# Performance work log

Measured on AMD Instinct MI355X. Metric: run time of the kernel, lower is better.

The kernel has to match this reference:

```python
import jax, jax.numpy as jnp
import numpy as np

NUM_USERS = 100000
NUM_ITEMS = 50000
EMB = 64
N_LAYERS = 3
N_EDGES = 2400000
NEG_SLOPE = 0.01  # torch F.leaky_relu default
EPS = 1e-12       # torch F.normalize default eps


def setup_inputs() -> dict:
    key = jax.random.key(0)
    ks = jax.random.split(key, 9)
    N = NUM_USERS + NUM_ITEMS
    adj_rows = jax.random.randint(ks[0], (N_EDGES,), 0, N, dtype=jnp.int32)
    adj_cols = jax.random.randint(ks[1], (N_EDGES,), 0, N, dtype=jnp.int32)
    # normalized adjacency values are small positive numbers
    adj_vals = jax.random.uniform(ks[2], (N_EDGES,), dtype=jnp.float32) * 0.01
    user_emb = jax.random.normal(ks[3], (NUM_USERS, EMB), dtype=jnp.float32) * 0.1
    item_emb = jax.random.normal(ks[4], (NUM_ITEMS, EMB), dtype=jnp.float32) * 0.1
    gc_w = jax.random.normal(ks[5], (N_LAYERS, EMB, EMB), dtype=jnp.float32) * 0.05
    gc_b = jax.random.normal(ks[6], (N_LAYERS, EMB), dtype=jnp.float32) * 0.01
    bi_w = jax.random.normal(ks[7], (N_LAYERS, EMB, EMB), dtype=jnp.float32) * 0.05
    bi_b = jax.random.normal(ks[8], (N_LAYERS, EMB), dtype=jnp.float32) * 0.01
    return {"adj_rows": adj_rows, "adj_cols": adj_cols, "adj_vals": adj_vals,
            "user_emb": user_emb, "item_emb": item_emb,
            "gc_w": gc_w, "gc_b": gc_b, "bi_w": bi_w, "bi_b": bi_b}


def reference(adj_rows, adj_cols, adj_vals, user_emb, item_emb, gc_w, gc_b, bi_w, bi_b):
    n_users = user_emb.shape[0]
    N = n_users + item_emb.shape[0]
    ego = jnp.concatenate([user_emb, item_emb], axis=0)  # [N, d]
    all_emb = [ego]
    n_layers = gc_w.shape[0]
    for i in range(n_layers):
        # SpMM: side = norm_adj @ ego  (COO gather-scale-scatter)
        side = jax.ops.segment_sum(adj_vals[:, None] * ego[adj_cols],
                                   adj_rows, num_segments=N)  # [N, d]
        sum_emb = jax.nn.leaky_relu(side @ gc_w[i] + gc_b[i], NEG_SLOPE)
        bi_emb = jax.nn.leaky_relu((ego * side) @ bi_w[i] + bi_b[i], NEG_SLOPE)
        ego = sum_emb + bi_emb  # dropout p=0 -> identity (eval mode)
        norm = ego / jnp.maximum(
            jnp.linalg.norm(ego, axis=1, keepdims=True), EPS)
        all_emb.append(norm)
    all_emb = jnp.concatenate(all_emb, axis=1)  # [N, d*(1+L)]
    return all_emb[:n_users], all_emb[n_users:]
```

## Files before the change

### kernel.cpp

```cpp
#include <hip/hip_runtime.h>
#include <hip/hip_bf16.h>

#define NUSERS 100000
#define NITEMS 50000
#define NNODES 150000
#define EMB 64
#define NLAYERS 3
#define NEDGES 2400000
#define SCAN_ITEMS 1024
#define NSCAN_BLOCKS ((NNODES + SCAN_ITEMS - 1) / SCAN_ITEMS)
#define NTILES (NNODES / 16)

typedef __attribute__((ext_vector_type(8))) short short8;
typedef __attribute__((ext_vector_type(4))) float float4v;

__device__ __forceinline__ float bf2f(unsigned short u) {
    return __uint_as_float((unsigned int)u << 16);
}
__device__ __forceinline__ unsigned short f2bf(float f) {
    unsigned int x = __float_as_uint(f);
    return (unsigned short)((x + 0x7FFFu + ((x >> 16) & 1u)) >> 16);
}


__global__ __launch_bounds__(256) void hist_rank_kernel(
    const int* __restrict__ rows, int* __restrict__ deg, int* __restrict__ rank)
{
    int e = blockIdx.x * 256 + threadIdx.x;
    if (e >= NEDGES) return;
    rank[e] = atomicAdd(&deg[rows[e]], 1);
}

__global__ __launch_bounds__(256) void block_sum_kernel(
    const int* __restrict__ deg, int* __restrict__ bsum)
{
    __shared__ int lds[256];
    int t = threadIdx.x;
    int base = blockIdx.x * SCAN_ITEMS + t * 4;
    int s = 0;
    #pragma unroll
    for (int k = 0; k < 4; ++k) {
        int idx = base + k;
        s += (idx < NNODES) ? deg[idx] : 0;
    }
    lds[t] = s; __syncthreads();
    for (int off = 128; off; off >>= 1) {
        if (t < off) lds[t] += lds[t + off];
        __syncthreads();
    }
    if (t == 0) bsum[blockIdx.x] = lds[0];
}

__global__ __launch_bounds__(256) void scan_partials_kernel(
    const int* __restrict__ bsum, int* __restrict__ bscan, int* __restrict__ rowptr)
{
    __shared__ int lds[256];
    int t = threadIdx.x;
    int v = (t < NSCAN_BLOCKS) ? bsum[t] : 0;
    lds[t] = v; __syncthreads();
    for (int off = 1; off < 256; off <<= 1) {
        int add = (t >= off) ? lds[t - off] : 0;
        __syncthreads();
        lds[t] += add;
        __syncthreads();
    }
    if (t < NSCAN_BLOCKS) bscan[t] = lds[t] - v;
    if (t == 0) rowptr[NNODES] = NEDGES;
}

__global__ __launch_bounds__(256) void block_scan_kernel(
    const int* __restrict__ deg, const int* __restrict__ bscan,
    int* __restrict__ rowptr)
{
    __shared__ int lds[256];
    int t = threadIdx.x;
    int base = blockIdx.x * SCAN_ITEMS + t * 4;
    int d[4]; int s = 0;
    #pragma unroll
    for (int k = 0; k < 4; ++k) {
        int idx = base + k;
        d[k] = (idx < NNODES) ? deg[idx] : 0;
        s += d[k];
    }
    lds[t] = s; __syncthreads();
    int v = s;
    for (int off = 1; off < 256; off <<= 1) {
        int add = (t >= off) ? lds[t - off] : 0;
        __syncthreads();
        lds[t] += add;
        __syncthreads();
    }
    int ex = lds[t] - v + bscan[blockIdx.x];
    #pragma unroll
    for (int k = 0; k < 4; ++k) {
        int idx = base + k;
        if (idx < NNODES) { rowptr[idx] = ex; ex += d[k]; }
    }
}

__global__ __launch_bounds__(256) void scatter_kernel(
    const int* __restrict__ rows, const int* __restrict__ cols,
    const float* __restrict__ vals, const int* __restrict__ rank,
    const int* __restrict__ rowptr, int2* __restrict__ edges)
{
    int e = blockIdx.x * 256 + threadIdx.x;
    if (e >= NEDGES) return;
    int pos = rowptr[rows[e]] + rank[e];
    edges[pos] = make_int2(cols[e], __float_as_int(vals[e]));
}

__global__ __launch_bounds__(256) void wconv_kernel(
    const float* __restrict__ gw, const float* __restrict__ bw,
    unsigned short* __restrict__ wg_bf, unsigned short* __restrict__ wb_bf)
{
    int i = blockIdx.x * 256 + threadIdx.x;
    if (i >= NLAYERS * EMB * EMB) return;
    int l = i >> 12;
    int k = (i >> 6) & 63;
    int n = i & 63;
    int o = (l << 12) | (n << 6) | k;
    wg_bf[o] = f2bf(gw[i]);
    wb_bf[o] = f2bf(bw[i]);
}

__global__ __launch_bounds__(256) void init_kernel(
    const float* __restrict__ ue, const float* __restrict__ ie,
    unsigned short* __restrict__ ego_bf, float* __restrict__ out)
{
    int i = blockIdx.x * 256 + threadIdx.x;
    if (i >= NNODES * 16) return;
    int n = i >> 4, q = i & 15;
    float4 v = (n < NUSERS) ? ((const float4*)ue)[i]
                            : ((const float4*)ie)[i - NUSERS * 16];
    *(float4*)(out + (size_t)n * 256 + q * 4) = v;
    ushort4 b;
    b.x = f2bf(v.x); b.y = f2bf(v.y); b.z = f2bf(v.z); b.w = f2bf(v.w);
    *(ushort4*)(ego_bf + (size_t)n * EMB + q * 4) = b;
}

__global__ __launch_bounds__(256) void spmm_pull(
    const int* __restrict__ rowptr, const int2* __restrict__ edges,
    const unsigned short* __restrict__ ego_bf, unsigned short* __restrict__ side_bf)
{
    const int t  = threadIdx.x;
    const int cp = t & 15;
    const int r  = blockIdx.x * 16 + (t >> 4);
    const int s = rowptr[r], e = rowptr[r + 1];

    float a0 = 0.f, a1 = 0.f, a2 = 0.f, a3 = 0.f;
    float b0 = 0.f, b1 = 0.f, b2 = 0.f, b3 = 0.f;
    int i = s;
    for (; i + 2 <= e; i += 2) {
        int2 e0 = edges[i];
        int2 e1 = edges[i + 1];
        float v0 = __int_as_float(e0.y);
        float v1 = __int_as_float(e1.y);
        uint2 u0 = *(const uint2*)(ego_bf + (size_t)e0.x * EMB + cp * 4);
        uint2 u1 = *(const uint2*)(ego_bf + (size_t)e1.x * EMB + cp * 4);
        a0 += v0 * __uint_as_float(u0.x << 16);
        a1 += v0 * __uint_as_float(u0.x & 0xffff0000u);
        a2 += v0 * __uint_as_float(u0.y << 16);
        a3 += v0 * __uint_as_float(u0.y & 0xffff0000u);
        b0 += v1 * __uint_as_float(u1.x << 16);
        b1 += v1 * __uint_as_float(u1.x & 0xffff0000u);
        b2 += v1 * __uint_as_float(u1.y << 16);
        b3 += v1 * __uint_as_float(u1.y & 0xffff0000u);
    }
    if (i < e) {
        int2 e0 = edges[i];
        float v0 = __int_as_float(e0.y);
        uint2 u0 = *(const uint2*)(ego_bf + (size_t)e0.x * EMB + cp * 4);
        a0 += v0 * __uint_as_float(u0.x << 16);
        a1 += v0 * __uint_as_float(u0.x & 0xffff0000u);
        a2 += v0 * __uint_as_float(u0.y << 16);
        a3 += v0 * __uint_as_float(u0.y & 0xffff0000u);
    }
    a0 += b0; a1 += b1; a2 += b2; a3 += b3;

    ushort4 o;
    o.x = f2bf(a0); o.y = f2bf(a1); o.z = f2bf(a2); o.w = f2bf(a3);
    *(ushort4*)(side_bf + (size_t)r * EMB + cp * 4) = o;
}

__global__ __launch_bounds__(256) void dense_mfma(
    const unsigned short* __restrict__ side_bf, unsigned short* __restrict__ ego_bf,
    const unsigned short* __restrict__ wg_bf, const unsigned short* __restrict__ wb_bf,
    const float* __restrict__ gb, const float* __restrict__ bb,
    float* __restrict__ out, int out_col0)
{
    const int lane = threadIdx.x & 63;
    const int w    = threadIdx.x >> 6;
    const int m    = lane & 15;
    const int q    = lane >> 4;

    const int t = (int)blockIdx.x * 4 + w;
    if (t >= NTILES) return;

    short8 bg[4][2], bbf[4][2];
    #pragma unroll
    for (int n0 = 0; n0 < 4; ++n0) {
        const int n = n0 * 16 + m;
        #pragma unroll
        for (int kh = 0; kh < 2; ++kh) {
            bg [n0][kh] = *(const short8*)(wg_bf + n * EMB + kh * 32 + q * 8);
            bbf[n0][kh] = *(const short8*)(wb_bf + n * EMB + kh * 32 + q * 8);
        }
    }
    float bgc[4], bbc[4];
    #pragma unroll
    for (int n0 = 0; n0 < 4; ++n0) { bgc[n0] = gb[n0 * 16 + m]; bbc[n0] = bb[n0 * 16 + m]; }

    const size_t base = (size_t)t * 16 * EMB;
    const int ao = m * EMB + q * 8;
    short8 as0 = *(const short8*)(side_bf + base + ao);
    short8 as1 = *(const short8*)(side_bf + base + ao + 32);
    short8 ae0 = *(const short8*)(ego_bf  + base + ao);
    short8 ae1 = *(const short8*)(ego_bf  + base + ao + 32);
    short8 ap0, ap1;
    #pragma unroll
    for (int jj = 0; jj < 8; ++jj) {
        ap0[jj] = (short)f2bf(bf2f((unsigned short)as0[jj]) * bf2f((unsigned short)ae0[jj]));
        ap1[jj] = (short)f2bf(bf2f((unsigned short)as1[jj]) * bf2f((unsigned short)ae1[jj]));
    }

    float4v c1[4], c2[4];
    #pragma unroll
    for (int n0 = 0; n0 < 4; ++n0) { c1[n0] = (float4v)0.f; c2[n0] = (float4v)0.f; }
    #pragma unroll
    for (int n0 = 0; n0 < 4; ++n0) {
        c1[n0] = __builtin_amdgcn_mfma_f32_16x16x32_bf16(as0, bg [n0][0], c1[n0], 0, 0, 0);
        c1[n0] = __builtin_amdgcn_mfma_f32_16x16x32_bf16(as1, bg [n0][1], c1[n0], 0, 0, 0);
        c2[n0] = __builtin_amdgcn_mfma_f32_16x16x32_bf16(ap0, bbf[n0][0], c2[n0], 0, 0, 0);
        c2[n0] = __builtin_amdgcn_mfma_f32_16x16x32_bf16(ap1, bbf[n0][1], c2[n0], 0, 0, 0);
    }

    float eg[4][4];
    float ss[4] = {0.f, 0.f, 0.f, 0.f};
    #pragma unroll
    for (int n0 = 0; n0 < 4; ++n0) {
        #pragma unroll
        for (int r = 0; r < 4; ++r) {
            float a1 = c1[n0][r] + bgc[n0];
            float a2 = c2[n0][r] + bbc[n0];
            float v1 = a1 > 0.f ? a1 : 0.01f * a1;
            float v2 = a2 > 0.f ? a2 : 0.01f * a2;
            float e = v1 + v2;
            eg[n0][r] = e;
            ss[r] += e * e;
        }
    }
    #pragma unroll
    for (int r = 0; r < 4; ++r) {
        float s = ss[r];
        s += __shfl_xor(s, 1, 64);
        s += __shfl_xor(s, 2, 64);
        s += __shfl_xor(s, 4, 64);
        s += __shfl_xor(s, 8, 64);
        ss[r] = 1.0f / fmaxf(sqrtf(s), 1e-12f);
    }
    #pragma unroll
    for (int r = 0; r < 4; ++r) {
        int row = t * 16 + q * 4 + r;
        #pragma unroll
        for (int n0 = 0; n0 < 4; ++n0) {
            int col = n0 * 16 + m;
            ego_bf[(size_t)row * EMB + col] = f2bf(eg[n0][r]);
            out[(size_t)row * 256 + out_col0 + col] = eg[n0][r] * ss[r];
        }
    }
}

extern "C" void kernel_launch(void* const* d_in, const int* in_sizes, int n_in,
                              void* d_out, int out_size, void* d_ws, size_t ws_size,
                              hipStream_t stream)
{
    const int*   rows = (const int*)  d_in[0];
    const int*   cols = (const int*)  d_in[1];
    const float* vals = (const float*)d_in[2];
    const float* ue   = (const float*)d_in[3];
    const float* ie   = (const float*)d_in[4];
    const float* gw   = (const float*)d_in[5];
    const float* gb   = (const float*)d_in[6];
    const float* bw   = (const float*)d_in[7];
    const float* bb   = (const float*)d_in[8];
    float* out = (float*)d_out;

    char* p = (char*)d_ws;
    unsigned short* ego_bf  = (unsigned short*)p;  p += (size_t)NNODES * EMB * 2;
    unsigned short* side_bf = (unsigned short*)p;  p += (size_t)NNODES * EMB * 2;
    int2*  edges  = (int2*)p;    p += (size_t)NEDGES * 8;
    int*   rowptr = (int*)p;     p += ((size_t)NNODES + 4) * 4;
    unsigned short* wg_bf = (unsigned short*)p;  p += (size_t)NLAYERS * EMB * EMB * 2;
    unsigned short* wb_bf = (unsigned short*)p;  p += (size_t)NLAYERS * EMB * EMB * 2;
    int* deg   = (int*)side_bf;
    int* rank  = (int*)side_bf + NNODES;
    int* bsum  = (int*)side_bf + NNODES + NEDGES;
    int* bscan = bsum + 256;

    hipMemsetAsync(deg, 0, (size_t)NNODES * 4, stream);
    hist_rank_kernel<<<(NEDGES + 255) / 256, 256, 0, stream>>>(rows, deg, rank);
    block_sum_kernel<<<NSCAN_BLOCKS, 256, 0, stream>>>(deg, bsum);
    scan_partials_kernel<<<1, 256, 0, stream>>>(bsum, bscan, rowptr);
    block_scan_kernel<<<NSCAN_BLOCKS, 256, 0, stream>>>(deg, bscan, rowptr);
    scatter_kernel<<<(NEDGES + 255) / 256, 256, 0, stream>>>(
        rows, cols, vals, rank, rowptr, edges);

    wconv_kernel<<<(NLAYERS * EMB * EMB + 255) / 256, 256, 0, stream>>>(gw, bw, wg_bf, wb_bf);
    init_kernel<<<(NNODES * 16 + 255) / 256, 256, 0, stream>>>(ue, ie, ego_bf, out);

    for (int l = 0; l < NLAYERS; ++l) {
        spmm_pull<<<NNODES / 16, 256, 0, stream>>>(rowptr, edges, ego_bf, side_bf);
        dense_mfma<<<(NTILES + 3) / 4, 256, 0, stream>>>(
            side_bf, ego_bf,
            wg_bf + l * EMB * EMB, wb_bf + l * EMB * EMB,
            gb + l * EMB, bb + l * EMB,
            out, 64 * (l + 1));
    }
}
```

Before: 632.3 us.

## Fuse SpMM and dense MFMA per layer, bucket degree histogram atomics

Each layer's SpMM pull and dense MFMA transform now run in one kernel: the aggregated side rows are staged in LDS rather than written to and re-read from global memory, and ego is ping-ponged between two buffers. The SpMM inner loop is unrolled to 4 edges. CSR construction splits the degree histogram into 8 buckets chosen by block index to reduce atomic contention, at the cost of an extra prefix kernel and a larger memset. Fusing the two stages raises register and LDS pressure and may lower occupancy during the gather phase.

```diff
diff --git a/kernel.cpp b/kernel.cpp
--- a/kernel.cpp
+++ b/kernel.cpp
@@ -9,7 +9,7 @@
 #define NEDGES 2400000
 #define SCAN_ITEMS 1024
 #define NSCAN_BLOCKS ((NNODES + SCAN_ITEMS - 1) / SCAN_ITEMS)
-#define NTILES (NNODES / 16)
+#define NBUCK 8
 
 typedef __attribute__((ext_vector_type(8))) short short8;
 typedef __attribute__((ext_vector_type(4))) float float4v;
@@ -21,14 +21,32 @@
     unsigned int x = __float_as_uint(f);
     return (unsigned short)((x + 0x7FFFu + ((x >> 16) & 1u)) >> 16);
 }
-
-
-__global__ __launch_bounds__(256) void hist_rank_kernel(
-    const int* __restrict__ rows, int* __restrict__ deg, int* __restrict__ rank)
+__device__ __forceinline__ float bfl(unsigned int u) { return __uint_as_float(u << 16); }
+__device__ __forceinline__ float bfh(unsigned int u) { return __uint_as_float(u & 0xffff0000u); }
+
+
+__global__ __launch_bounds__(256) void hist8_kernel(
+    const int* __restrict__ rows, int* __restrict__ deg8, int* __restrict__ rank)
 {
     int e = blockIdx.x * 256 + threadIdx.x;
     if (e >= NEDGES) return;
-    rank[e] = atomicAdd(&deg[rows[e]], 1);
+    int b = blockIdx.x & (NBUCK - 1);
+    rank[e] = atomicAdd(&deg8[b * NNODES + rows[e]], 1);
+}
+
+__global__ __launch_bounds__(256) void bucket_prefix_kernel(
+    int* __restrict__ deg8, int* __restrict__ deg_tot)
+{
+    int i = blockIdx.x * 256 + threadIdx.x;
+    if (i >= NNODES) return;
+    int s = 0;
+    #pragma unroll
+    for (int b = 0; b < NBUCK; ++b) {
+        int v = deg8[b * NNODES + i];
+        deg8[b * NNODES + i] = s;
+        s += v;
+    }
+    deg_tot[i] = s;
 }
 
 __global__ __launch_bounds__(256) void block_sum_kernel(
@@ -98,14 +116,17 @@
     }
 }
 
-__global__ __launch_bounds__(256) void scatter_kernel(
+__global__ __launch_bounds__(256) void scatter8_kernel(
     const int* __restrict__ rows, const int* __restrict__ cols,
     const float* __restrict__ vals, const int* __restrict__ rank,
-    const int* __restrict__ rowptr, int2* __restrict__ edges)
+    const int* __restrict__ rowptr, const int* __restrict__ pre8,
+    int2* __restrict__ edges)
 {
     int e = blockIdx.x * 256 + threadIdx.x;
     if (e >= NEDGES) return;
-    int pos = rowptr[rows[e]] + rank[e];
+    int b = blockIdx.x & (NBUCK - 1);
+    int row = rows[e];
+    int pos = rowptr[row] + pre8[b * NNODES + row] + rank[e];
     edges[pos] = make_int2(cols[e], __float_as_int(vals[e]));
 }
 
@@ -138,63 +159,67 @@
     *(ushort4*)(ego_bf + (size_t)n * EMB + q * 4) = b;
 }
 
-__global__ __launch_bounds__(256) void spmm_pull(
+__global__ __launch_bounds__(256) void layer_fused(
     const int* __restrict__ rowptr, const int2* __restrict__ edges,
-    const unsigned short* __restrict__ ego_bf, unsigned short* __restrict__ side_bf)
-{
-    const int t  = threadIdx.x;
-    const int cp = t & 15;
-    const int r  = blockIdx.x * 16 + (t >> 4);
-    const int s = rowptr[r], e = rowptr[r + 1];
-
-    float a0 = 0.f, a1 = 0.f, a2 = 0.f, a3 = 0.f;
-    float b0 = 0.f, b1 = 0.f, b2 = 0.f, b3 = 0.f;
-    int i = s;
-    for (; i + 2 <= e; i += 2) {
-        int2 e0 = edges[i];
-        int2 e1 = edges[i + 1];
-        float v0 = __int_as_float(e0.y);
-        float v1 = __int_as_float(e1.y);
-        uint2 u0 = *(const uint2*)(ego_bf + (size_t)e0.x * EMB + cp * 4);
-        uint2 u1 = *(const uint2*)(ego_bf + (size_t)e1.x * EMB + cp * 4);
-        a0 += v0 * __uint_as_float(u0.x << 16);
-        a1 += v0 * __uint_as_float(u0.x & 0xffff0000u);
-        a2 += v0 * __uint_as_float(u0.y << 16);
-        a3 += v0 * __uint_as_float(u0.y & 0xffff0000u);
-        b0 += v1 * __uint_as_float(u1.x << 16);
-        b1 += v1 * __uint_as_float(u1.x & 0xffff0000u);
-        b2 += v1 * __uint_as_float(u1.y << 16);
-        b3 += v1 * __uint_as_float(u1.y & 0xffff0000u);
-    }
-    if (i < e) {
-        int2 e0 = edges[i];
-        float v0 = __int_as_float(e0.y);
-        uint2 u0 = *(const uint2*)(ego_bf + (size_t)e0.x * EMB + cp * 4);
-        a0 += v0 * __uint_as_float(u0.x << 16);
-        a1 += v0 * __uint_as_float(u0.x & 0xffff0000u);
-        a2 += v0 * __uint_as_float(u0.y << 16);
-        a3 += v0 * __uint_as_float(u0.y & 0xffff0000u);
-    }
-    a0 += b0; a1 += b1; a2 += b2; a3 += b3;
-
-    ushort4 o;
-    o.x = f2bf(a0); o.y = f2bf(a1); o.z = f2bf(a2); o.w = f2bf(a3);
-    *(ushort4*)(side_bf + (size_t)r * EMB + cp * 4) = o;
-}
-
-__global__ __launch_bounds__(256) void dense_mfma(
-    const unsigned short* __restrict__ side_bf, unsigned short* __restrict__ ego_bf,
+    const unsigned short* __restrict__ ego_in, unsigned short* __restrict__ ego_out,
     const unsigned short* __restrict__ wg_bf, const unsigned short* __restrict__ wb_bf,
     const float* __restrict__ gb, const float* __restrict__ bb,
     float* __restrict__ out, int out_col0)
 {
-    const int lane = threadIdx.x & 63;
-    const int w    = threadIdx.x >> 6;
+    __shared__ unsigned short lds_side[4][16][72];
+
+    const int t    = threadIdx.x;
+    const int cp   = t & 15;
+    const int g    = t >> 4;
+    const int base = (int)blockIdx.x * 64;
+
+    #pragma unroll
+    for (int k = 0; k < 4; ++k) {
+        int r = base + k * 16 + g;
+        if (r < NNODES) {
+            const int s = rowptr[r], e = rowptr[r + 1];
+            float a0 = 0.f, a1 = 0.f, a2 = 0.f, a3 = 0.f;
+            float b0 = 0.f, b1 = 0.f, b2 = 0.f, b3 = 0.f;
+            int i = s;
+            for (; i + 4 <= e; i += 4) {
+                int2 e0 = edges[i],     e1 = edges[i + 1];
+                int2 e2 = edges[i + 2], e3 = edges[i + 3];
+                uint2 u0 = *(const uint2*)(ego_in + (size_t)e0.x * EMB + cp * 4);
+                uint2 u1 = *(const uint2*)(ego_in + (size_t)e1.x * EMB + cp * 4);
+                uint2 u2 = *(const uint2*)(ego_in + (size_t)e2.x * EMB + cp * 4);
+                uint2 u3 = *(const uint2*)(ego_in + (size_t)e3.x * EMB + cp * 4);
+                float v0 = __int_as_float(e0.y), v1 = __int_as_float(e1.y);
+                float v2 = __int_as_float(e2.y), v3 = __int_as_float(e3.y);
+                a0 += v0 * bfl(u0.x); a1 += v0 * bfh(u0.x);
+                a2 += v0 * bfl(u0.y); a3 += v0 * bfh(u0.y);
+                b0 += v1 * bfl(u1.x); b1 += v1 * bfh(u1.x);
+                b2 += v1 * bfl(u1.y); b3 += v1 * bfh(u1.y);
+                a0 += v2 * bfl(u2.x); a1 += v2 * bfh(u2.x);
+                a2 += v2 * bfl(u2.y); a3 += v2 * bfh(u2.y);
+                b0 += v3 * bfl(u3.x); b1 += v3 * bfh(u3.x);
+                b2 += v3 * bfl(u3.y); b3 += v3 * bfh(u3.y);
+            }
+            for (; i < e; ++i) {
+                int2 e0 = edges[i];
+                float v0 = __int_as_float(e0.y);
+                uint2 u0 = *(const uint2*)(ego_in + (size_t)e0.x * EMB + cp * 4);
+                a0 += v0 * bfl(u0.x); a1 += v0 * bfh(u0.x);
+                a2 += v0 * bfl(u0.y); a3 += v0 * bfh(u0.y);
+            }
+            a0 += b0; a1 += b1; a2 += b2; a3 += b3;
+            ushort4 o;
+            o.x = f2bf(a0); o.y = f2bf(a1); o.z = f2bf(a2); o.w = f2bf(a3);
+            *(ushort4*)&lds_side[k][g][cp * 4] = o;
+        }
+    }
+    __syncthreads();
+
+    const int lane = t & 63;
+    const int w    = t >> 6;
     const int m    = lane & 15;
     const int q    = lane >> 4;
-
-    const int t = (int)blockIdx.x * 4 + w;
-    if (t >= NTILES) return;
+    const int tb   = base + w * 16;
+    if (tb >= NNODES) return;
 
     short8 bg[4][2], bbf[4][2];
     #pragma unroll
@@ -210,12 +235,10 @@
     #pragma unroll
     for (int n0 = 0; n0 < 4; ++n0) { bgc[n0] = gb[n0 * 16 + m]; bbc[n0] = bb[n0 * 16 + m]; }
 
-    const size_t base = (size_t)t * 16 * EMB;
-    const int ao = m * EMB + q * 8;
-    short8 as0 = *(const short8*)(side_bf + base + ao);
-    short8 as1 = *(const short8*)(side_bf + base + ao + 32);
-    short8 ae0 = *(const short8*)(ego_bf  + base + ao);
-    short8 ae1 = *(const short8*)(ego_bf  + base + ao + 32);
+    short8 as0 = *(const short8*)&lds_side[w][m][q * 8];
+    short8 as1 = *(const short8*)&lds_side[w][m][q * 8 + 32];
+    short8 ae0 = *(const short8*)(ego_in + (size_t)(tb + m) * EMB + q * 8);
+    short8 ae1 = *(const short8*)(ego_in + (size_t)(tb + m) * EMB + q * 8 + 32);
     short8 ap0, ap1;
     #pragma unroll
     for (int jj = 0; jj < 8; ++jj) {
@@ -240,10 +263,10 @@
     for (int n0 = 0; n0 < 4; ++n0) {
         #pragma unroll
         for (int r = 0; r < 4; ++r) {
-            float a1 = c1[n0][r] + bgc[n0];
-            float a2 = c2[n0][r] + bbc[n0];
-            float v1 = a1 > 0.f ? a1 : 0.01f * a1;
-            float v2 = a2 > 0.f ? a2 : 0.01f * a2;
+            float x1 = c1[n0][r] + bgc[n0];
+            float x2 = c2[n0][r] + bbc[n0];
+            float v1 = x1 > 0.f ? x1 : 0.01f * x1;
+            float v2 = x2 > 0.f ? x2 : 0.01f * x2;
             float e = v1 + v2;
             eg[n0][r] = e;
             ss[r] += e * e;
@@ -260,11 +283,11 @@
     }
     #pragma unroll
     for (int r = 0; r < 4; ++r) {
-        int row = t * 16 + q * 4 + r;
+        int row = tb + q * 4 + r;
         #pragma unroll
         for (int n0 = 0; n0 < 4; ++n0) {
             int col = n0 * 16 + m;
-            ego_bf[(size_t)row * EMB + col] = f2bf(eg[n0][r]);
+            ego_out[(size_t)row * EMB + col] = f2bf(eg[n0][r]);
             out[(size_t)row * 256 + out_col0 + col] = eg[n0][r] * ss[r];
         }
     }
@@ -286,32 +309,35 @@
     float* out = (float*)d_out;
 
     char* p = (char*)d_ws;
-    unsigned short* ego_bf  = (unsigned short*)p;  p += (size_t)NNODES * EMB * 2;
-    unsigned short* side_bf = (unsigned short*)p;  p += (size_t)NNODES * EMB * 2;
+    unsigned short* ego0 = (unsigned short*)p;  p += (size_t)NNODES * EMB * 2;
+    unsigned short* ego1 = (unsigned short*)p;  p += (size_t)NNODES * EMB * 2;
     int2*  edges  = (int2*)p;    p += (size_t)NEDGES * 8;
     int*   rowptr = (int*)p;     p += ((size_t)NNODES + 4) * 4;
     unsigned short* wg_bf = (unsigned short*)p;  p += (size_t)NLAYERS * EMB * EMB * 2;
     unsigned short* wb_bf = (unsigned short*)p;  p += (size_t)NLAYERS * EMB * EMB * 2;
-    int* deg   = (int*)side_bf;
-    int* rank  = (int*)side_bf + NNODES;
-    int* bsum  = (int*)side_bf + NNODES + NEDGES;
-    int* bscan = bsum + 256;
-
-    hipMemsetAsync(deg, 0, (size_t)NNODES * 4, stream);
-    hist_rank_kernel<<<(NEDGES + 255) / 256, 256, 0, stream>>>(rows, deg, rank);
-    block_sum_kernel<<<NSCAN_BLOCKS, 256, 0, stream>>>(deg, bsum);
+    int* deg8    = (int*)ego1;
+    int* rank    = deg8 + NBUCK * NNODES;
+    int* deg_tot = rank + NEDGES;
+    int* bsum    = deg_tot + NNODES;
+    int* bscan   = bsum + 256;
+
+    hipMemsetAsync(deg8, 0, (size_t)NBUCK * NNODES * 4, stream);
+    hist8_kernel<<<(NEDGES + 255) / 256, 256, 0, stream>>>(rows, deg8, rank);
+    bucket_prefix_kernel<<<(NNODES + 255) / 256, 256, 0, stream>>>(deg8, deg_tot);
+    block_sum_kernel<<<NSCAN_BLOCKS, 256, 0, stream>>>(deg_tot, bsum);
     scan_partials_kernel<<<1, 256, 0, stream>>>(bsum, bscan, rowptr);
-    block_scan_kernel<<<NSCAN_BLOCKS, 256, 0, stream>>>(deg, bscan, rowptr);
-    scatter_kernel<<<(NEDGES + 255) / 256, 256, 0, stream>>>(
-        rows, cols, vals, rank, rowptr, edges);
+    block_scan_kernel<<<NSCAN_BLOCKS, 256, 0, stream>>>(deg_tot, bscan, rowptr);
+    scatter8_kernel<<<(NEDGES + 255) / 256, 256, 0, stream>>>(
+        rows, cols, vals, rank, rowptr, deg8, edges);
 
     wconv_kernel<<<(NLAYERS * EMB * EMB + 255) / 256, 256, 0, stream>>>(gw, bw, wg_bf, wb_bf);
-    init_kernel<<<(NNODES * 16 + 255) / 256, 256, 0, stream>>>(ue, ie, ego_bf, out);
+    init_kernel<<<(NNODES * 16 + 255) / 256, 256, 0, stream>>>(ue, ie, ego0, out);
 
     for (int l = 0; l < NLAYERS; ++l) {
-        spmm_pull<<<NNODES / 16, 256, 0, stream>>>(rowptr, edges, ego_bf, side_bf);
-        dense_mfma<<<(NTILES + 3) / 4, 256, 0, stream>>>(
-            side_bf, ego_bf,
+        const unsigned short* ein = (l & 1) ? ego1 : ego0;
+        unsigned short*       eout = (l & 1) ? ego0 : ego1;
+        layer_fused<<<(NNODES + 63) / 64, 256, 0, stream>>>(
+            rowptr, edges, ein, eout,
             wg_bf + l * EMB * EMB, wb_bf + l * EMB * EMB,
             gb + l * EMB, bb + l * EMB,
             out, 64 * (l + 1));
```

New measurement: 688.2 us. 8.8% more time.
